# Kernel tuning notes

Hardware: AMD Instinct MI355X
Metric: run time of the kernel (lower is better)

## Reference

```python
import jax, jax.numpy as jnp
import numpy as np

B, T, C, H = 4, 2048, 768, 12
D = C // H  # head dim = 64


def setup_inputs() -> dict:
    key = jax.random.key(0)
    ks = jax.random.split(key, 4)
    scale = 0.02
    return {
        "x": jax.random.normal(ks[0], (B, T, C), dtype=jnp.float32),
        "W_attn": jax.random.normal(ks[1], (C, 3 * C), dtype=jnp.float32) * scale,
        "b_attn": jnp.zeros((3 * C,), dtype=jnp.float32),
        "W_proj": jax.random.normal(ks[2], (C, C), dtype=jnp.float32) * scale,
        "b_proj": jnp.zeros((C,), dtype=jnp.float32),
    }


def reference(x, W_attn, b_attn, W_proj, b_proj):
    Bsz, Tlen, Cdim = x.shape
    qkv = x @ W_attn + b_attn                    # [B,T,3C]
    q, k, v = jnp.split(qkv, 3, axis=-1)          # each [B,T,C]
    # [B,T,C] -> [B,H,T,D]
    def heads(t):
        return t.reshape(Bsz, Tlen, H, D).transpose(0, 2, 1, 3)
    q, k, v = heads(q), heads(k), heads(v)
    att = jnp.einsum("bhqd,bhkd->bhqk", q, k) * (1.0 / np.sqrt(D))
    # causal mask: position q attends to k <= q
    mask = jnp.tril(jnp.ones((Tlen, Tlen), dtype=bool))
    att = jnp.where(mask[None, None], att, -jnp.inf)
    att = jax.nn.softmax(att, axis=-1)
    y = jnp.einsum("bhqk,bhkd->bhqd", att, v)     # [B,H,T,D]
    y = y.transpose(0, 2, 1, 3).reshape(Bsz, Tlen, Cdim)
    return y @ W_proj + b_proj
```

## Files before the change

kernel.cpp:

```cpp
#include <hip/hip_runtime.h>

#define B_SZ   4
#define T_LEN  2048
#define C_DIM  768
#define H_NUM  12
#define THREEC (3 * C_DIM)

typedef _Float16 f16;
typedef _Float16 half8 __attribute__((ext_vector_type(8)));
typedef _Float16 half4 __attribute__((ext_vector_type(4)));
typedef float    f32x4 __attribute__((ext_vector_type(4)));

#define GLD16(gaddr, laddr)                                                         \
  __builtin_amdgcn_global_load_lds(                                                 \
      (const __attribute__((address_space(1))) unsigned int*)(gaddr),               \
      (__attribute__((address_space(3))) unsigned int*)(laddr), 16, 0, 0)
#define MFMA16(a, b, c) __builtin_amdgcn_mfma_f32_16x16x32_f16(a, b, c, 0, 0, 0)

__global__ __launch_bounds__(256) void cast_f32_f16_kernel(
    const float* __restrict__ src, f16* __restrict__ dst, int n8) {
  int i = blockIdx.x * 256 + threadIdx.x;
  if (i >= n8) return;
  const float* s = src + (size_t)i * 8;
  half8 h;
#pragma unroll
  for (int u = 0; u < 8; ++u) h[u] = (f16)s[u];
  *(half8*)(dst + (size_t)i * 8) = h;
}

__global__ __launch_bounds__(256) void transpose_cast2_kernel(
    const float* __restrict__ Wa, const float* __restrict__ Wp,
    f16* __restrict__ WtA, f16* __restrict__ WtP) {
  __shared__ f16 tile[32][33];
  int bx = blockIdx.x;
  const float* W; f16* Wt; int N;
  if (bx < THREEC / 32) { W = Wa; Wt = WtA; N = THREEC; }
  else { W = Wp; Wt = WtP; N = C_DIM; bx -= THREEC / 32; }
  const int n0 = bx * 32, k0 = blockIdx.y * 32;
  const int tx = threadIdx.x & 31, ty = threadIdx.x >> 5;
#pragma unroll
  for (int i = 0; i < 4; ++i)
    tile[ty + i * 8][tx] = (f16)W[(size_t)(k0 + ty + i * 8) * N + n0 + tx];
  __syncthreads();
#pragma unroll
  for (int i = 0; i < 4; ++i)
    Wt[(size_t)(n0 + ty + i * 8) * C_DIM + k0 + tx] = tile[tx][ty + i * 8];
}

template <int BM, int BN, int OUT_F16>
__global__ __launch_bounds__(256) void gemm_f16_kernel(
    const f16* __restrict__ A, const f16* __restrict__ Bt,
    const float* __restrict__ bias, f16* __restrict__ OutH,
    float* __restrict__ OutF, int M, int N, int K) {
  __shared__ f16 As[BM * 64];
  __shared__ f16 Bs[BN * 64];
  const int tid = threadIdx.x;
  const int lane = tid & 63, wave = tid >> 6;
  const int lm = lane & 15, kq = lane >> 4, lm7 = lm & 7;
  constexpr int MT = BM / 32, NT = BN / 32;
  const int wm = (wave & 1) * (BM / 2), wn = (wave >> 1) * (BN / 2);
  const int row0 = blockIdx.y * BM, col0 = blockIdx.x * BN;

  f32x4 acc[MT][NT] = {};

  for (int k0 = 0; k0 < K; k0 += 64) {
    __syncthreads();
#pragma unroll
    for (int i = 0; i < BM / 32; ++i) {
      int c = tid + i * 256;
      int r = c >> 3, cc = (c & 7) ^ (r & 7);
      GLD16(&A[(size_t)(row0 + r) * K + k0 + cc * 8],
            &As[(i * 256 + wave * 64) * 8]);
    }
#pragma unroll
    for (int i = 0; i < BN / 32; ++i) {
      int c = tid + i * 256;
      int r = c >> 3, cc = (c & 7) ^ (r & 7);
      GLD16(&Bt[(size_t)(col0 + r) * K + k0 + cc * 8],
            &Bs[(i * 256 + wave * 64) * 8]);
    }
    __syncthreads();
#pragma unroll
    for (int ks = 0; ks < 2; ++ks) {
      const int pos = (ks * 4 + kq);
      half8 af[MT], bf[NT];
#pragma unroll
      for (int t = 0; t < MT; ++t)
        af[t] = *(const half8*)&As[(wm + t * 16 + lm) * 64 + (pos ^ lm7) * 8];
#pragma unroll
      for (int t = 0; t < NT; ++t)
        bf[t] = *(const half8*)&Bs[(wn + t * 16 + lm) * 64 + (pos ^ lm7) * 8];
#pragma unroll
      for (int mt = 0; mt < MT; ++mt)
#pragma unroll
        for (int nt = 0; nt < NT; ++nt)
          acc[mt][nt] = MFMA16(af[mt], bf[nt], acc[mt][nt]);
    }
  }

#pragma unroll
  for (int mt = 0; mt < MT; ++mt) {
    const int row = row0 + wm + mt * 16 + kq * 4;
#pragma unroll
    for (int nt = 0; nt < NT; ++nt) {
      const int col = col0 + wn + nt * 16 + lm;
      const float bv = bias[col];
#pragma unroll
      for (int r = 0; r < 4; ++r) {
        float v = acc[mt][nt][r] + bv;
        if (OUT_F16)
          OutH[(size_t)(row + r) * N + col] = (f16)v;
        else
          OutF[(size_t)(row + r) * N + col] = v;
      }
    }
  }
}

__global__ __launch_bounds__(256) void v_transpose_kernel(
    const f16* __restrict__ qkv, f16* __restrict__ vt) {
  __shared__ f16 tile[64 * 68];
  const int bh = blockIdx.x, b = bh / H_NUM, h = bh % H_NUM;
  const int t0 = blockIdx.y * 64;
  const int tid = threadIdx.x;
#pragma unroll
  for (int i = 0; i < 2; ++i) {
    int c = tid + i * 256;
    int tr = c >> 3, doff = (c & 7) * 8;
    half8 v = *(const half8*)&qkv[(size_t)(b * T_LEN + t0 + tr) * THREEC + 2 * C_DIM + h * 64 + doff];
#pragma unroll
    for (int u = 0; u < 8; ++u) tile[(doff + u) * 68 + tr] = v[u];
  }
  __syncthreads();
#pragma unroll
  for (int i = 0; i < 2; ++i) {
    int c = tid + i * 256;
    int d = c >> 3, toff = (c & 7) * 8;
    half8 v;
#pragma unroll
    for (int u = 0; u < 8; ++u) v[u] = tile[d * 68 + toff + u];
    *(half8*)&vt[((size_t)bh * 64 + d) * T_LEN + t0 + toff] = v;
  }
}

__global__ __launch_bounds__(512, 6) void attn_kernel(
    const f16* __restrict__ qkv, const f16* __restrict__ vt,
    f16* __restrict__ y) {
  __shared__ f16 Kt[64 * 64];
  __shared__ f16 Vt[64 * 64];
  __shared__ f16 Pl[8][16 * 64];

  const int bh = blockIdx.x, b = bh / H_NUM, h = bh % H_NUM;
  const int yb = blockIdx.y;
  const int tid = threadIdx.x, lane = tid & 63, wave = tid >> 6;
  const int lm = lane & 15, kq = lane >> 4, lm7 = lm & 7;
  const int cw = (wave < 4) ? (31 - yb) : yb;
  const int qw = cw * 64 + (wave & 3) * 16;
  const f16 qscale = (f16)(0.125f * 1.44269504f);

  half8 vones;
#pragma unroll
  for (int u = 0; u < 8; ++u) vones[u] = (f16)1.f;

  half8 bq[2];
#pragma unroll
  for (int c2 = 0; c2 < 2; ++c2) {
    half8 v = *(const half8*)&qkv[(size_t)(b * T_LEN + qw + lm) * THREEC +
                                  h * 64 + c2 * 32 + kq * 8];
    bq[c2] = v * qscale;
  }

  f32x4 o[4] = {};
  f32x4 ol = {};

  const int srow = tid >> 3;
  const int scol = ((tid & 7) ^ (srow & 7)) * 8;
  const f16* kp = &qkv[(size_t)(b * T_LEN + srow) * THREEC + C_DIM + h * 64 + scol];
  const f16* vp = &vt[((size_t)bh * 64 + srow) * T_LEN + scol];

  f16* prow = &Pl[wave][lm * 64];

  const int n_tiles = 32 - yb;
  for (int it = 0; it < n_tiles; ++it) {
    __syncthreads();
    GLD16(kp, &Kt[(wave * 64) * 8]);
    kp += (size_t)64 * THREEC;
    GLD16(vp, &Vt[(wave * 64) * 8]);
    vp += 64;
    __syncthreads();

    if (it <= cw) {
      f32x4 s4[4];
#pragma unroll
      for (int ct = 0; ct < 4; ++ct) {
        const f16* kr = &Kt[(ct * 16 + lm) * 64];
        half8 ak0 = *(const half8*)&kr[(kq ^ lm7) * 8];
        half8 ak1 = *(const half8*)&kr[((4 + kq) ^ lm7) * 8];
        f32x4 z = {};
        z = MFMA16(ak0, bq[0], z);
        s4[ct] = MFMA16(ak1, bq[1], z);
      }
      if (it == cw) {
        const int qrow = qw + lm, j0 = it * 64;
#pragma unroll
        for (int ct = 0; ct < 4; ++ct)
#pragma unroll
          for (int r = 0; r < 4; ++r)
            if (j0 + ct * 16 + kq * 4 + r > qrow) s4[ct][r] = -1e30f;
      }
#pragma unroll
      for (int ct = 0; ct < 4; ++ct) {
        half4 pk;
#pragma unroll
        for (int r = 0; r < 4; ++r) pk[r] = (f16)exp2f(s4[ct][r]);
        *(half4*)&prow[(((ct * 2 + (kq >> 1)) ^ lm7) * 8) + (kq & 1) * 4] = pk;
      }
      __asm__ volatile("s_waitcnt lgkmcnt(0)" ::: "memory");
      half8 ap0 = *(const half8*)&prow[(kq ^ lm7) * 8];
      half8 ap1 = *(const half8*)&prow[((4 + kq) ^ lm7) * 8];
#pragma unroll
      for (int dt = 0; dt < 4; ++dt) {
        const f16* vr = &Vt[(dt * 16 + lm) * 64];
        half8 bv0 = *(const half8*)&vr[(kq ^ lm7) * 8];
        half8 bv1 = *(const half8*)&vr[((4 + kq) ^ lm7) * 8];
        o[dt] = MFMA16(ap0, bv0, o[dt]);
        o[dt] = MFMA16(ap1, bv1, o[dt]);
      }
      ol = MFMA16(ap0, vones, ol);
      ol = MFMA16(ap1, vones, ol);
    }
  }

#pragma unroll
  for (int r = 0; r < 4; ++r) {
    const float inv = 1.f / ol[r];
    const size_t base =
        (size_t)(b * T_LEN + qw + kq * 4 + r) * C_DIM + h * 64;
#pragma unroll
    for (int dt = 0; dt < 4; ++dt)
      y[base + dt * 16 + lm] = (f16)(o[dt][r] * inv);
  }
}

extern "C" void kernel_launch(void* const* d_in, const int* in_sizes, int n_in,
                              void* d_out, int out_size, void* d_ws, size_t ws_size,
                              hipStream_t stream) {
  const float* x      = (const float*)d_in[0];
  const float* W_attn = (const float*)d_in[1];
  const float* b_attn = (const float*)d_in[2];
  const float* W_proj = (const float*)d_in[3];
  const float* b_proj = (const float*)d_in[4];
  float* out = (float*)d_out;

  const int M = B_SZ * T_LEN;
  auto align256 = [](size_t v) { return (v + 255) & ~(size_t)255; };
  char* ws = (char*)d_ws;
  f16* xh   = (f16*)ws; ws += align256((size_t)M * C_DIM * 2);
  f16* WtA  = (f16*)ws; ws += align256((size_t)THREEC * C_DIM * 2);
  f16* WtP  = (f16*)ws; ws += align256((size_t)C_DIM * C_DIM * 2);
  f16* qkvh = (f16*)ws; ws += align256((size_t)M * THREEC * 2);
  f16* vtg  = (f16*)ws; ws += align256((size_t)B_SZ * H_NUM * 64 * T_LEN * 2);
  f16* yh   = (f16*)ws; ws += align256((size_t)M * C_DIM * 2);

  {
    int n8 = M * C_DIM / 8;
    cast_f32_f16_kernel<<<(n8 + 255) / 256, 256, 0, stream>>>(x, xh, n8);
  }
  transpose_cast2_kernel<<<dim3((THREEC + C_DIM) / 32, C_DIM / 32), 256, 0, stream>>>(
      W_attn, W_proj, WtA, WtP);

  gemm_f16_kernel<128, 128, 1><<<dim3(THREEC / 128, M / 128), 256, 0, stream>>>(
      xh, WtA, b_attn, qkvh, nullptr, M, THREEC, C_DIM);

  v_transpose_kernel<<<dim3(B_SZ * H_NUM, T_LEN / 64), 256, 0, stream>>>(qkvh, vtg);

  attn_kernel<<<dim3(B_SZ * H_NUM, 16), 512, 0, stream>>>(qkvh, vtg, yh);

  gemm_f16_kernel<128, 64, 0><<<dim3(C_DIM / 64, M / 128), 256, 0, stream>>>(
      yh, WtP, b_proj, nullptr, out, M, C_DIM, C_DIM);
}
```

Before: 211.7 us.

## Double-buffer K/V tiles in attention and use raw exp2 with packed f16 convert

The attention loop now keeps two LDS buffers for K and V. It issues the global-to-LDS load for the next tile before computing on the current one, and syncs with an explicit vmcnt wait and s_barrier, so load latency overlaps with the MFMA work. It also swaps exp2f plus scalar f16 casts for the raw exp2 builtin and packed round-toward-zero conversion, and reuses a pinned zero accumulator. LDS use grows by 16KB per block, which may lower occupancy under the 6-blocks launch bound, and RTZ rounding changes precision slightly.

Result: faster. 196.2 us (-7.3%).

```diff
diff --git a/kernel.cpp b/kernel.cpp
--- a/kernel.cpp
+++ b/kernel.cpp
@@ -9,6 +9,7 @@
 typedef _Float16 f16;
 typedef _Float16 half8 __attribute__((ext_vector_type(8)));
 typedef _Float16 half4 __attribute__((ext_vector_type(4)));
+typedef __fp16   pk2   __attribute__((ext_vector_type(2)));
 typedef float    f32x4 __attribute__((ext_vector_type(4)));
 
 #define GLD16(gaddr, laddr)                                                         \
@@ -146,8 +147,8 @@
 __global__ __launch_bounds__(512, 6) void attn_kernel(
     const f16* __restrict__ qkv, const f16* __restrict__ vt,
     f16* __restrict__ y) {
-  __shared__ f16 Kt[64 * 64];
-  __shared__ f16 Vt[64 * 64];
+  __shared__ f16 Kt[2][64 * 64];
+  __shared__ f16 Vt[2][64 * 64];
   __shared__ f16 Pl[8][16 * 64];
 
   const int bh = blockIdx.x, b = bh / H_NUM, h = bh % H_NUM;
@@ -173,31 +174,45 @@
   f32x4 o[4] = {};
   f32x4 ol = {};
 
+  f32x4 fz = {};
+  asm volatile("" : "+v"(fz));
+
   const int srow = tid >> 3;
   const int scol = ((tid & 7) ^ (srow & 7)) * 8;
   const f16* kp = &qkv[(size_t)(b * T_LEN + srow) * THREEC + C_DIM + h * 64 + scol];
   const f16* vp = &vt[((size_t)bh * 64 + srow) * T_LEN + scol];
 
   f16* prow = &Pl[wave][lm * 64];
+  const int sbase = wave * 512;
 
   const int n_tiles = 32 - yb;
+
+  GLD16(kp, &Kt[0][sbase]);
+  kp += (size_t)64 * THREEC;
+  GLD16(vp, &Vt[0][sbase]);
+  vp += 64;
+
   for (int it = 0; it < n_tiles; ++it) {
-    __syncthreads();
-    GLD16(kp, &Kt[(wave * 64) * 8]);
-    kp += (size_t)64 * THREEC;
-    GLD16(vp, &Vt[(wave * 64) * 8]);
-    vp += 64;
-    __syncthreads();
+    const int cur = it & 1;
+    if (it + 1 < n_tiles) {
+      GLD16(kp, &Kt[cur ^ 1][sbase]);
+      kp += (size_t)64 * THREEC;
+      GLD16(vp, &Vt[cur ^ 1][sbase]);
+      vp += 64;
+      asm volatile("s_waitcnt vmcnt(2)" ::: "memory");
+    } else {
+      asm volatile("s_waitcnt vmcnt(0)" ::: "memory");
+    }
+    __builtin_amdgcn_s_barrier();
 
     if (it <= cw) {
       f32x4 s4[4];
 #pragma unroll
       for (int ct = 0; ct < 4; ++ct) {
-        const f16* kr = &Kt[(ct * 16 + lm) * 64];
+        const f16* kr = &Kt[cur][(ct * 16 + lm) * 64];
         half8 ak0 = *(const half8*)&kr[(kq ^ lm7) * 8];
         half8 ak1 = *(const half8*)&kr[((4 + kq) ^ lm7) * 8];
-        f32x4 z = {};
-        z = MFMA16(ak0, bq[0], z);
+        f32x4 z = MFMA16(ak0, bq[0], fz);
         s4[ct] = MFMA16(ak1, bq[1], z);
       }
       if (it == cw) {
@@ -210,17 +225,19 @@
       }
 #pragma unroll
       for (int ct = 0; ct < 4; ++ct) {
-        half4 pk;
-#pragma unroll
-        for (int r = 0; r < 4; ++r) pk[r] = (f16)exp2f(s4[ct][r]);
-        *(half4*)&prow[(((ct * 2 + (kq >> 1)) ^ lm7) * 8) + (kq & 1) * 4] = pk;
+        union { half4 h4; pk2 p2[2]; } u;
+        u.p2[0] = __builtin_amdgcn_cvt_pkrtz(
+            __builtin_amdgcn_exp2f(s4[ct][0]), __builtin_amdgcn_exp2f(s4[ct][1]));
+        u.p2[1] = __builtin_amdgcn_cvt_pkrtz(
+            __builtin_amdgcn_exp2f(s4[ct][2]), __builtin_amdgcn_exp2f(s4[ct][3]));
+        *(half4*)&prow[(((ct * 2 + (kq >> 1)) ^ lm7) * 8) + (kq & 1) * 4] = u.h4;
       }
       __asm__ volatile("s_waitcnt lgkmcnt(0)" ::: "memory");
       half8 ap0 = *(const half8*)&prow[(kq ^ lm7) * 8];
       half8 ap1 = *(const half8*)&prow[((4 + kq) ^ lm7) * 8];
 #pragma unroll
       for (int dt = 0; dt < 4; ++dt) {
-        const f16* vr = &Vt[(dt * 16 + lm) * 64];
+        const f16* vr = &Vt[cur][(dt * 16 + lm) * 64];
         half8 bv0 = *(const half8*)&vr[(kq ^ lm7) * 8];
         half8 bv1 = *(const half8*)&vr[((4 + kq) ^ lm7) * 8];
         o[dt] = MFMA16(ap0, bv0, o[dt]);
@@ -229,6 +246,8 @@
       ol = MFMA16(ap0, vones, ol);
       ol = MFMA16(ap1, vones, ol);
     }
+
+    __builtin_amdgcn_s_barrier();
   }
 
 #pragma unroll
```
